# Kernel tuning notes

Hardware: AMD Instinct MI355X
Metric: run time of the kernel (lower is better)

The kernel has to match this reference:

```python
import jax, jax.numpy as jnp
import numpy as np

EPS = 1e-05
HEADS = 4

def rms_norm(x, w):
    norm = jax.lax.rsqrt(jnp.mean(x * x, axis=-1, keepdims=True) + EPS)
    return x * norm * w

def setup_inputs() -> dict:
    key = jax.random.key(0)
    ks = jax.random.split(key, 10)
    B, Nt, Nf, C = 2, 4096, 4096, 256
    s = 0.02
    return {
        "t": jax.random.normal(ks[0], (B, Nt, C), jnp.float32),
        "f": jax.random.normal(ks[1], (B, Nf, C), jnp.float32),
        "norm_w": jnp.ones((C,), jnp.float32),
        "wq": jax.random.normal(ks[2], (C, C), jnp.float32) * s,
        "bq": jnp.zeros((C,), jnp.float32),
        "wkv": jax.random.normal(ks[3], (C, 2 * C), jnp.float32) * s,
        "bkv": jnp.zeros((2 * C,), jnp.float32),
        "wp": jax.random.normal(ks[4], (C, C), jnp.float32) * s,
        "bp": jnp.zeros((C,), jnp.float32),
    }

def reference(t, f, norm_w, wq, bq, wkv, bkv, wp, bp):
    B, Nt, C = t.shape
    Nf = f.shape[1]
    H = HEADS
    Dh = C // H
    scale = Dh ** -0.5
    tn = rms_norm(t, norm_w)
    fn = rms_norm(f, norm_w)
    q = (tn @ wq + bq).reshape(B, Nt, H, Dh)          # b t h d
    kv = fn @ wkv + bkv
    k, v = jnp.split(kv, 2, axis=-1)
    k = k.reshape(B, Nf, H, Dh)                        # b f h d
    v = v.reshape(B, Nf, H, Dh)
    attn = jnp.einsum('bthd,bfhd->bhtf', q, k) * scale
    attn = jax.nn.softmax(attn, axis=-1)
    out = jnp.einsum('bhtf,bfhd->bthd', attn, v).reshape(B, Nt, C)
    return out @ wp + bp + tn
```

## Files before the change

kernel.cpp:

```cpp
#include <hip/hip_runtime.h>

typedef __bf16 bf16;
typedef __bf16 bf16x4 __attribute__((ext_vector_type(4)));
typedef __bf16 bf16x8 __attribute__((ext_vector_type(8)));
typedef float f32x2 __attribute__((ext_vector_type(2)));
typedef float f32x4 __attribute__((ext_vector_type(4)));
typedef float f32x16 __attribute__((ext_vector_type(16)));

__device__ __forceinline__ f32x4 mfma16(bf16x8 a, bf16x8 b, f32x4 c) {
  return __builtin_amdgcn_mfma_f32_16x16x32_bf16(a, b, c, 0, 0, 0);
}
__device__ __forceinline__ f32x16 mfma32(bf16x8 a, bf16x8 b, f32x16 c) {
  return __builtin_amdgcn_mfma_f32_32x32x16_bf16(a, b, c, 0, 0, 0);
}

__device__ __forceinline__ unsigned pack2(float lo, float hi) {
  unsigned short a = __builtin_bit_cast(unsigned short, (bf16)lo);
  unsigned short b = __builtin_bit_cast(unsigned short, (bf16)hi);
  return ((unsigned)b << 16) | (unsigned)a;
}

__device__ __forceinline__ void plane32swap(unsigned& a, unsigned& b) {
  asm volatile("v_permlane32_swap_b32 %0, %1" : "+v"(a), "+v"(b));
}

__device__ __forceinline__ f32x2 pk_add(f32x2 a, f32x2 b) {
  f32x2 d;
  asm("v_pk_add_f32 %0, %1, %2" : "=v"(d) : "v"(a), "v"(b));
  return d;
}

typedef __attribute__((address_space(3))) unsigned int lds_u32;
typedef __attribute__((address_space(1))) unsigned int glb_u32;
__device__ __forceinline__ void gld16(const bf16* g, bf16* l) {
  __builtin_amdgcn_global_load_lds((const glb_u32*)g, (lds_u32*)l, 16, 0, 0);
}

__global__ __launch_bounds__(256)
void prep_kernel(const float* __restrict__ t, const float* __restrict__ f,
                 const float* __restrict__ nw,
                 const float* __restrict__ wq, const float* __restrict__ wkv,
                 const float* __restrict__ wp,
                 bf16* __restrict__ tn, bf16* __restrict__ fn,
                 bf16* __restrict__ wqT, bf16* __restrict__ wkvT,
                 bf16* __restrict__ wpT)
{
  int b = blockIdx.x;
  if (b < 1024) {
    int e = b * 256 + threadIdx.x;
    const float* src; bf16* dst; int N; int idx;
    if (e < 65536)       { src = wq;  dst = wqT;  N = 256; idx = e; }
    else if (e < 196608) { src = wkv; dst = wkvT; N = 512; idx = e - 65536; }
    else                 { src = wp;  dst = wpT;  N = 256; idx = e - 196608; }
    int k = idx & 255;
    int n = idx >> 8;
    dst[idx] = (bf16)src[(size_t)k * N + n];
    return;
  }
  int wave = threadIdx.x >> 6;
  int lane = threadIdx.x & 63;
  int row = (b - 1024) * 4 + wave;
  const float* src;
  bf16* dst;
  if (row < 8192) {
    src = t + (size_t)row * 256;
    dst = tn + (size_t)row * 256;
  } else {
    int r2 = row - 8192;
    src = f + (size_t)r2 * 256;
    dst = fn + (size_t)r2 * 256;
  }
  float4 v = reinterpret_cast<const float4*>(src)[lane];
  float ss = v.x * v.x + v.y * v.y + v.z * v.z + v.w * v.w;
  #pragma unroll
  for (int m = 1; m < 64; m <<= 1) ss += __shfl_xor(ss, m);
  float nrm = rsqrtf(ss * (1.0f / 256.0f) + 1e-5f);
  float4 wv = reinterpret_cast<const float4*>(nw)[lane];
  bf16x4 o;
  o[0] = (bf16)(v.x * nrm * wv.x);
  o[1] = (bf16)(v.y * nrm * wv.y);
  o[2] = (bf16)(v.z * nrm * wv.z);
  o[3] = (bf16)(v.w * nrm * wv.w);
  *reinterpret_cast<bf16x4*>(dst + lane * 4) = o;
}

template<int MODE>
__device__ __forceinline__
void gemm_body(int bid, bf16 (*As)[264], bf16 (*Bs)[264],
               const bf16* __restrict__ A, const bf16* __restrict__ Wt,
               const float* __restrict__ bias, bf16* __restrict__ o0,
               bf16* __restrict__ o1, const bf16* __restrict__ resid,
               float* __restrict__ outf, int N)
{
  int tid = threadIdx.x;
  int wv = tid >> 6;
  int lane = tid & 63;
  int lr = lane & 15;
  int lk = (lane >> 4) * 8;
  int wm = wv >> 1, wn = wv & 1;
  int nb = N >> 6;
  int bm = bid / nb;
  int bn = bid - bm * nb;
  int row0 = bm * 64;
  int col0 = bn * 64;

  #pragma unroll
  for (int j = 0; j < 8; j++) {
    int idx = tid + 256 * j;
    int r = idx >> 5, ch = idx & 31;
    *reinterpret_cast<bf16x8*>(&As[r][ch * 8]) =
        *reinterpret_cast<const bf16x8*>(A + (size_t)(row0 + r) * 256 + ch * 8);
    *reinterpret_cast<bf16x8*>(&Bs[r][ch * 8]) =
        *reinterpret_cast<const bf16x8*>(Wt + (size_t)(col0 + r) * 256 + ch * 8);
  }
  __syncthreads();

  f32x4 acc[2][2] = {};
  #pragma unroll
  for (int k0 = 0; k0 < 256; k0 += 32) {
    bf16x8 a[2], b[2];
    #pragma unroll
    for (int mi = 0; mi < 2; mi++)
      a[mi] = *reinterpret_cast<const bf16x8*>(&As[wm * 32 + mi * 16 + lr][k0 + lk]);
    #pragma unroll
    for (int ni = 0; ni < 2; ni++)
      b[ni] = *reinterpret_cast<const bf16x8*>(&Bs[wn * 32 + ni * 16 + lr][k0 + lk]);
    #pragma unroll
    for (int mi = 0; mi < 2; mi++)
      #pragma unroll
      for (int ni = 0; ni < 2; ni++)
        acc[mi][ni] = mfma16(a[mi], b[ni], acc[mi][ni]);
  }

  int rb = (lane >> 4) * 4;
  int row0w = row0 + wm * 32;
  int col0w = col0 + wn * 32;
  #pragma unroll
  for (int mi = 0; mi < 2; mi++) {
    #pragma unroll
    for (int ni = 0; ni < 2; ni++) {
      int col = col0w + ni * 16 + lr;
      float bv = bias[col];
      #pragma unroll
      for (int r = 0; r < 4; r++) {
        int row = row0w + mi * 16 + rb + r;
        float val = acc[mi][ni][r] + bv;
        if (MODE == 0) {
          int b_ = row >> 12, tt = row & 4095;
          int h = col >> 6, d = col & 63;
          o0[(((size_t)(b_ * 4 + h)) * 4096 + tt) * 64 + d] = (bf16)val;
        } else if (MODE == 1) {
          int b_ = row >> 12, ff = row & 4095;
          if (col < 256) {
            int h = col >> 6, d = col & 63;
            o0[(((size_t)(b_ * 4 + h)) * 4096 + ff) * 64 + d] = (bf16)val;
          } else {
            int c = col - 256;
            int h = c >> 6, d = c & 63;
            o1[(((size_t)(b_ * 4 + h)) * 64 + d) * 4096 + ff] = (bf16)val;
          }
        } else {
          size_t idx = (size_t)row * 256 + col;
          outf[idx] = val + (float)resid[idx];
        }
      }
    }
  }
}

__global__ __launch_bounds__(256)
void gemm_qkv(const bf16* __restrict__ tn, const bf16* __restrict__ fn,
              const bf16* __restrict__ wqT, const bf16* __restrict__ wkvT,
              const float* __restrict__ bq, const float* __restrict__ bkv,
              bf16* __restrict__ q, bf16* __restrict__ k, bf16* __restrict__ vt)
{
  __shared__ bf16 As[64][264];
  __shared__ bf16 Bs[64][264];
  if (blockIdx.x < 512)
    gemm_body<0>(blockIdx.x, As, Bs, tn, wqT, bq, q, nullptr, nullptr, nullptr, 256);
  else
    gemm_body<1>(blockIdx.x - 512, As, Bs, fn, wkvT, bkv, k, vt, nullptr, nullptr, 512);
}

__global__ __launch_bounds__(256)
void gemm_out(const bf16* __restrict__ ao, const bf16* __restrict__ wpT,
              const float* __restrict__ bp, const bf16* __restrict__ resid,
              float* __restrict__ outf)
{
  __shared__ bf16 As[64][264];
  __shared__ bf16 Bs[64][264];
  gemm_body<2>(blockIdx.x, As, Bs, ao, wpT, bp, nullptr, nullptr, resid, outf, 256);
}

__global__ __launch_bounds__(128, 4)
void attn_kernel(const bf16* __restrict__ Q, const bf16* __restrict__ K,
                 const bf16* __restrict__ Vt, unsigned* __restrict__ Opart,
                 float* __restrict__ Lp)
{
  int bid = blockIdx.x;
  int bh = bid & 7;
  int qb = (bid >> 3) & 63;
  int FQ = bid >> 9;
  int wv = threadIdx.x >> 6;
  int lane = threadIdx.x & 63;
  int lq = lane & 31;
  int h32 = lane >> 5;

  const bf16* Qb = Q + ((size_t)bh * 4096 + qb * 64 + wv * 32) * 64;
  const bf16* Kb = K + (size_t)bh * 4096 * 64;
  const bf16* Vb = Vt + (size_t)bh * 64 * 4096;

  __shared__ bf16 stage[2][4096];

  const float qs = 0.125f * 1.44269504089f;
  bf16x8 qf[4];
  #pragma unroll
  for (int kc = 0; kc < 4; kc++) {
    qf[kc] = *reinterpret_cast<const bf16x8*>(Qb + (size_t)lq * 64 + kc * 16 + h32 * 8);
    #pragma unroll
    for (int i = 0; i < 8; i++) qf[kc][i] = (bf16)((float)qf[kc][i] * qs);
  }

  f32x16 zmm = {};
  f32x16 oa[2] = {};
  float l = 0.f;

  int fbeg = FQ * 1024;

  const bf16 *p0, *p1;
  if (wv == 0) {
    p0 = Kb + (size_t)(fbeg + lq) * 64 + h32 * 8;
    p1 = p0 + 32 * 64;
  } else {
    p0 = Vb + (size_t)lane * 4096 + fbeg;
    p1 = p0 + 32;
  }

  const bf16* kL0 = &stage[0][0] + h32 * 256 + lq * 8;
  const bf16* kL1 = &stage[1][0] + h32 * 256 + lq * 8;
  const bf16* vL0 = &stage[0][2048] + h32 * 512 + lq * 8;
  const bf16* vL1 = &stage[1][2048] + h32 * 512 + lq * 8;

  auto STAGE = [&](bf16* sb, const bf16* p) {
    if (wv == 0) {
      gld16(p,      sb);
      gld16(p + 16, sb + 512);
      gld16(p + 32, sb + 1024);
      gld16(p + 48, sb + 1536);
    } else {
      gld16(p,      sb + 2048);
      gld16(p + 8,  sb + 2560);
      gld16(p + 16, sb + 3072);
      gld16(p + 24, sb + 3584);
    }
  };

  auto BODY = [&](const bf16* kL, const bf16* vL) {
    asm volatile("s_waitcnt vmcnt(4)" ::: "memory");
    __builtin_amdgcn_s_barrier();
    asm volatile("" ::: "memory");

    f32x16 st = mfma32(*reinterpret_cast<const bf16x8*>(kL),        qf[0], zmm);
    st        = mfma32(*reinterpret_cast<const bf16x8*>(kL + 512),  qf[1], st);
    st        = mfma32(*reinterpret_cast<const bf16x8*>(kL + 1024), qf[2], st);
    st        = mfma32(*reinterpret_cast<const bf16x8*>(kL + 1536), qf[3], st);

    union { f32x2 p2[8]; float s[16]; } u;
    #pragma unroll
    for (int r = 0; r < 16; r++) u.s[r] = exp2f(st[r]);

    f32x2 a0 = pk_add(u.p2[0], u.p2[1]);
    f32x2 a1 = pk_add(u.p2[2], u.p2[3]);
    f32x2 a2 = pk_add(u.p2[4], u.p2[5]);
    f32x2 a3 = pk_add(u.p2[6], u.p2[7]);
    a0 = pk_add(a0, a1);
    a2 = pk_add(a2, a3);
    a0 = pk_add(a0, a2);
    l += a0[0] + a0[1];

    unsigned w[8];
    #pragma unroll
    for (int j = 0; j < 8; j++) w[j] = pack2(u.s[2 * j], u.s[2 * j + 1]);
    plane32swap(w[0], w[2]);
    plane32swap(w[1], w[3]);
    plane32swap(w[4], w[6]);
    plane32swap(w[5], w[7]);
    union { unsigned u4[4]; bf16x8 v; } ub0, ub1;
    ub0.u4[0] = w[0]; ub0.u4[1] = w[1]; ub0.u4[2] = w[2]; ub0.u4[3] = w[3];
    ub1.u4[0] = w[4]; ub1.u4[1] = w[5]; ub1.u4[2] = w[6]; ub1.u4[3] = w[7];

    oa[0] = mfma32(*reinterpret_cast<const bf16x8*>(vL),        ub0.v, oa[0]);
    oa[0] = mfma32(*reinterpret_cast<const bf16x8*>(vL + 1024), ub1.v, oa[0]);
    oa[1] = mfma32(*reinterpret_cast<const bf16x8*>(vL + 256),  ub0.v, oa[1]);
    oa[1] = mfma32(*reinterpret_cast<const bf16x8*>(vL + 1280), ub1.v, oa[1]);

    asm volatile("" ::: "memory");
    __builtin_amdgcn_s_barrier();
    asm volatile("" ::: "memory");
  };

  STAGE(&stage[0][0], p0);
  STAGE(&stage[1][0], p1);
  asm volatile("" ::: "memory");

  const int adv = (wv == 0) ? 64 * 64 : 64;
  #pragma unroll 1
  for (int u = 0; u < 16; ++u) {
    BODY(kL0, vL0);
    p0 += adv;
    STAGE(&stage[0][0], p0);
    asm volatile("" ::: "memory");
    BODY(kL1, vL1);
    p1 += adv;
    STAGE(&stage[1][0], p1);
    asm volatile("" ::: "memory");
  }

  asm volatile("s_waitcnt vmcnt(0)" ::: "memory");

  float ltot;
  {
    unsigned x = __builtin_bit_cast(unsigned, l), y = x;
    plane32swap(x, y);
    ltot = __builtin_bit_cast(float, x) + __builtin_bit_cast(float, y);
  }

  unsigned* op = Opart + (((size_t)(FQ * 8 + bh) * 128 + qb * 2 + wv) * 1024);
  #pragma unroll
  for (int db = 0; db < 2; db++)
    #pragma unroll
    for (int j = 0; j < 8; j++) {
      int r = 2 * j;
      int d = db * 32 + 2 * (j & 1) + 8 * (j >> 1) + 4 * h32;
      op[(d >> 1) * 32 + lq] = pack2(oa[db][r], oa[db][r + 1]);
    }
  if (h32 == 0)
    Lp[((size_t)FQ * 8 + bh) * 4096 + qb * 64 + wv * 32 + lq] = ltot;
}

__global__ __launch_bounds__(256)
void merge_kernel(const unsigned* __restrict__ Op, const float* __restrict__ Lp,
                  bf16* __restrict__ AO)
{
  int bid = blockIdx.x;
  int bh = bid & 7;
  int tile = bid >> 3;
  int tid = threadIdx.x;
  int q = tid & 31;
  int c4 = tid >> 5;
  int row0 = tile * 32;

  float L = 0.f;
  #pragma unroll
  for (int p = 0; p < 4; p++)
    L += Lp[((size_t)p * 8 + bh) * 4096 + row0 + q];
  float inv = 1.f / L;

  __shared__ unsigned tl[32][33];
  float a0[4] = {}, a1[4] = {};
  #pragma unroll
  for (int p = 0; p < 4; p++) {
    const unsigned* src = Op + (((size_t)p * 8 + bh) * 128 + tile) * 1024;
    #pragma unroll
    for (int j = 0; j < 4; j++) {
      unsigned v = src[(c4 + j * 8) * 32 + q];
      a0[j] += (float)__builtin_bit_cast(bf16, (unsigned short)(v & 0xffff));
      a1[j] += (float)__builtin_bit_cast(bf16, (unsigned short)(v >> 16));
    }
  }
  #pragma unroll
  for (int j = 0; j < 4; j++)
    tl[q][c4 + j * 8] = pack2(a0[j] * inv, a1[j] * inv);
  __syncthreads();

  int q2 = tid >> 3;
  int dg = tid & 7;
  unsigned ov[4];
  #pragma unroll
  for (int i = 0; i < 4; i++) ov[i] = tl[q2][dg * 4 + i];
  int b_ = bh >> 2, hh = bh & 3;
  int row = row0 + q2;
  unsigned* dst = (unsigned*)(AO + ((size_t)b_ * 4096 + row) * 256 + hh * 64) + dg * 4;
  *reinterpret_cast<uint4*>(dst) = *reinterpret_cast<const uint4*>(ov);
}

extern "C" void kernel_launch(void* const* d_in, const int* in_sizes, int n_in,
                              void* d_out, int out_size, void* d_ws, size_t ws_size,
                              hipStream_t stream) {
  const float* t   = (const float*)d_in[0];
  const float* f   = (const float*)d_in[1];
  const float* nw  = (const float*)d_in[2];
  const float* wq  = (const float*)d_in[3];
  const float* bq  = (const float*)d_in[4];
  const float* wkv = (const float*)d_in[5];
  const float* bkv = (const float*)d_in[6];
  const float* wp  = (const float*)d_in[7];
  const float* bp  = (const float*)d_in[8];
  float* out = (float*)d_out;

  bf16* ws = (bf16*)d_ws;
  const size_t NTOK = 2097152;
  bf16* tn   = ws;
  bf16* fn   = ws + NTOK;
  bf16* q    = ws + 2 * NTOK;
  bf16* k    = ws + 3 * NTOK;
  bf16* vt   = ws + 4 * NTOK;
  bf16* ao   = fn;
  bf16* wqT  = ws + 5 * NTOK;
  bf16* wkvT = wqT + 65536;
  bf16* wpT  = wkvT + 131072;
  unsigned* opart = (unsigned*)(wpT + 65536);
  float* lp = (float*)(opart + (size_t)4 * 8 * 128 * 1024);

  prep_kernel<<<5120, 256, 0, stream>>>(t, f, nw, wq, wkv, wp, tn, fn, wqT, wkvT, wpT);
  gemm_qkv<<<1536, 256, 0, stream>>>(tn, fn, wqT, wkvT, bq, bkv, q, k, vt);
  attn_kernel<<<2048, 128, 0, stream>>>(q, k, vt, opart, lp);
  merge_kernel<<<1024, 256, 0, stream>>>(opart, lp, ao);
  gemm_out<<<512, 256, 0, stream>>>(ao, wpT, bp, tn, out);
}
```

Measured before the change: 110.8 us.

## Widen attention blocks to four waves sharing K/V staging, split keys eight ways

Each attention block now holds four waves covering 128 query rows instead of two covering 64, and all four waves share the staging of K and V tiles, so every wave issues two loads per stage instead of four. The key dimension is split into eight partitions of 512 instead of four of 1024, which keeps the grid at 2048 blocks. The goal is to halve K/V global and LDS staging traffic per query row and spread the loads across more waves. In exchange the merge kernel reads twice as many partial outputs, and the partial buffer doubles in size.

```diff
diff --git a/kernel.cpp b/kernel.cpp
--- a/kernel.cpp
+++ b/kernel.cpp
@@ -192,21 +192,21 @@
   gemm_body<2>(blockIdx.x, As, Bs, ao, wpT, bp, nullptr, nullptr, resid, outf, 256);
 }
 
-__global__ __launch_bounds__(128, 4)
+__global__ __launch_bounds__(256, 4)
 void attn_kernel(const bf16* __restrict__ Q, const bf16* __restrict__ K,
                  const bf16* __restrict__ Vt, unsigned* __restrict__ Opart,
                  float* __restrict__ Lp)
 {
   int bid = blockIdx.x;
   int bh = bid & 7;
-  int qb = (bid >> 3) & 63;
-  int FQ = bid >> 9;
+  int qb = (bid >> 3) & 31;
+  int FQ = bid >> 8;
   int wv = threadIdx.x >> 6;
   int lane = threadIdx.x & 63;
   int lq = lane & 31;
   int h32 = lane >> 5;
 
-  const bf16* Qb = Q + ((size_t)bh * 4096 + qb * 64 + wv * 32) * 64;
+  const bf16* Qb = Q + ((size_t)bh * 4096 + qb * 128 + wv * 32) * 64;
   const bf16* Kb = K + (size_t)bh * 4096 * 64;
   const bf16* Vb = Vt + (size_t)bh * 64 * 4096;
 
@@ -225,16 +225,21 @@
   f32x16 oa[2] = {};
   float l = 0.f;
 
-  int fbeg = FQ * 1024;
-
+  int fbeg = FQ * 512;
+
+  int role = wv >> 1;
+  int half = wv & 1;
   const bf16 *p0, *p1;
-  if (wv == 0) {
-    p0 = Kb + (size_t)(fbeg + lq) * 64 + h32 * 8;
+  if (role == 0) {
+    p0 = Kb + (size_t)(fbeg + lq) * 64 + h32 * 8 + half * 32;
     p1 = p0 + 32 * 64;
   } else {
-    p0 = Vb + (size_t)lane * 4096 + fbeg;
+    p0 = Vb + (size_t)lane * 4096 + fbeg + half * 16;
     p1 = p0 + 32;
   }
+  const int so  = role ? 8 : 16;
+  const int adv = role ? 64 : 64 * 64;
+  const int db0 = wv * 1024;
 
   const bf16* kL0 = &stage[0][0] + h32 * 256 + lq * 8;
   const bf16* kL1 = &stage[1][0] + h32 * 256 + lq * 8;
@@ -242,21 +247,12 @@
   const bf16* vL1 = &stage[1][2048] + h32 * 512 + lq * 8;
 
   auto STAGE = [&](bf16* sb, const bf16* p) {
-    if (wv == 0) {
-      gld16(p,      sb);
-      gld16(p + 16, sb + 512);
-      gld16(p + 32, sb + 1024);
-      gld16(p + 48, sb + 1536);
-    } else {
-      gld16(p,      sb + 2048);
-      gld16(p + 8,  sb + 2560);
-      gld16(p + 16, sb + 3072);
-      gld16(p + 24, sb + 3584);
-    }
+    gld16(p,      sb + db0);
+    gld16(p + so, sb + db0 + 512);
   };
 
   auto BODY = [&](const bf16* kL, const bf16* vL) {
-    asm volatile("s_waitcnt vmcnt(4)" ::: "memory");
+    asm volatile("s_waitcnt vmcnt(2)" ::: "memory");
     __builtin_amdgcn_s_barrier();
     asm volatile("" ::: "memory");
 
@@ -303,9 +299,8 @@
   STAGE(&stage[1][0], p1);
   asm volatile("" ::: "memory");
 
-  const int adv = (wv == 0) ? 64 * 64 : 64;
   #pragma unroll 1
-  for (int u = 0; u < 16; ++u) {
+  for (int u = 0; u < 8; ++u) {
     BODY(kL0, vL0);
     p0 += adv;
     STAGE(&stage[0][0], p0);
@@ -325,7 +320,8 @@
     ltot = __builtin_bit_cast(float, x) + __builtin_bit_cast(float, y);
   }
 
-  unsigned* op = Opart + (((size_t)(FQ * 8 + bh) * 128 + qb * 2 + wv) * 1024);
+  int tile = qb * 4 + wv;
+  unsigned* op = Opart + (((size_t)(FQ * 8 + bh) * 128 + tile) * 1024);
   #pragma unroll
   for (int db = 0; db < 2; db++)
     #pragma unroll
@@ -335,7 +331,7 @@
       op[(d >> 1) * 32 + lq] = pack2(oa[db][r], oa[db][r + 1]);
     }
   if (h32 == 0)
-    Lp[((size_t)FQ * 8 + bh) * 4096 + qb * 64 + wv * 32 + lq] = ltot;
+    Lp[((size_t)FQ * 8 + bh) * 4096 + tile * 32 + lq] = ltot;
 }
 
 __global__ __launch_bounds__(256)
@@ -352,14 +348,14 @@
 
   float L = 0.f;
   #pragma unroll
-  for (int p = 0; p < 4; p++)
+  for (int p = 0; p < 8; p++)
     L += Lp[((size_t)p * 8 + bh) * 4096 + row0 + q];
   float inv = 1.f / L;
 
   __shared__ unsigned tl[32][33];
   float a0[4] = {}, a1[4] = {};
   #pragma unroll
-  for (int p = 0; p < 4; p++) {
+  for (int p = 0; p < 8; p++) {
     const unsigned* src = Op + (((size_t)p * 8 + bh) * 128 + tile) * 1024;
     #pragma unroll
     for (int j = 0; j < 4; j++) {
@@ -410,11 +406,11 @@
   bf16* wkvT = wqT + 65536;
   bf16* wpT  = wkvT + 131072;
   unsigned* opart = (unsigned*)(wpT + 65536);
-  float* lp = (float*)(opart + (size_t)4 * 8 * 128 * 1024);
+  float* lp = (float*)(opart + (size_t)8 * 8 * 128 * 1024);
 
   prep_kernel<<<5120, 256, 0, stream>>>(t, f, nw, wq, wkv, wp, tn, fn, wqT, wkvT, wpT);
   gemm_qkv<<<1536, 256, 0, stream>>>(tn, fn, wqT, wkvT, bq, bkv, q, k, vt);
-  attn_kernel<<<2048, 128, 0, stream>>>(q, k, vt, opart, lp);
+  attn_kernel<<<2048, 256, 0, stream>>>(q, k, vt, opart, lp);
   merge_kernel<<<1024, 256, 0, stream>>>(opart, lp, ao);
   gemm_out<<<512, 256, 0, stream>>>(ao, wpT, bp, tn, out);
 }
```

After: 99.39 us. 10.3% less time.

## Process two query tiles per wave and split keys eight ways in attention

Applied to the files above, without the earlier changes.

Each attention wave now handles 64 query rows, as two 32-row tiles, against every staged K/V chunk. This doubles reuse of each LDS-staged key/value tile and halves the number of staging barriers per unit of work. To keep the grid the same size, the key range is split into 8 partitions instead of 4, so the merge kernel sums more partials and the partial buffer doubles. Launch bounds drop to 3 blocks per CU to allow for the extra registers, and the bf16 packing of probabilities now uses a single hardware convert-pack instruction.

```diff
diff --git a/kernel.cpp b/kernel.cpp
--- a/kernel.cpp
+++ b/kernel.cpp
@@ -18,6 +18,12 @@
   unsigned short a = __builtin_bit_cast(unsigned short, (bf16)lo);
   unsigned short b = __builtin_bit_cast(unsigned short, (bf16)hi);
   return ((unsigned)b << 16) | (unsigned)a;
+}
+
+__device__ __forceinline__ unsigned cvtpk(float lo, float hi) {
+  unsigned r;
+  asm("v_cvt_pk_bf16_f32 %0, %1, %2" : "=v"(r) : "v"(lo), "v"(hi));
+  return r;
 }
 
 __device__ __forceinline__ void plane32swap(unsigned& a, unsigned& b) {
@@ -192,40 +198,44 @@
   gemm_body<2>(blockIdx.x, As, Bs, ao, wpT, bp, nullptr, nullptr, resid, outf, 256);
 }
 
-__global__ __launch_bounds__(128, 4)
+__global__ __launch_bounds__(128, 3)
 void attn_kernel(const bf16* __restrict__ Q, const bf16* __restrict__ K,
                  const bf16* __restrict__ Vt, unsigned* __restrict__ Opart,
                  float* __restrict__ Lp)
 {
   int bid = blockIdx.x;
   int bh = bid & 7;
-  int qb = (bid >> 3) & 63;
-  int FQ = bid >> 9;
+  int qb = (bid >> 3) & 31;
+  int FQ = bid >> 8;
   int wv = threadIdx.x >> 6;
   int lane = threadIdx.x & 63;
   int lq = lane & 31;
   int h32 = lane >> 5;
 
-  const bf16* Qb = Q + ((size_t)bh * 4096 + qb * 64 + wv * 32) * 64;
+  const bf16* Qw = Q + ((size_t)bh * 4096 + qb * 128 + wv * 64) * 64;
   const bf16* Kb = K + (size_t)bh * 4096 * 64;
   const bf16* Vb = Vt + (size_t)bh * 64 * 4096;
 
   __shared__ bf16 stage[2][4096];
 
   const float qs = 0.125f * 1.44269504089f;
-  bf16x8 qf[4];
+  bf16x8 qfA[4], qfB[4];
   #pragma unroll
   for (int kc = 0; kc < 4; kc++) {
-    qf[kc] = *reinterpret_cast<const bf16x8*>(Qb + (size_t)lq * 64 + kc * 16 + h32 * 8);
-    #pragma unroll
-    for (int i = 0; i < 8; i++) qf[kc][i] = (bf16)((float)qf[kc][i] * qs);
+    qfA[kc] = *reinterpret_cast<const bf16x8*>(Qw + (size_t)lq * 64 + kc * 16 + h32 * 8);
+    qfB[kc] = *reinterpret_cast<const bf16x8*>(Qw + (size_t)(32 + lq) * 64 + kc * 16 + h32 * 8);
+    #pragma unroll
+    for (int i = 0; i < 8; i++) {
+      qfA[kc][i] = (bf16)((float)qfA[kc][i] * qs);
+      qfB[kc][i] = (bf16)((float)qfB[kc][i] * qs);
+    }
   }
 
   f32x16 zmm = {};
-  f32x16 oa[2] = {};
-  float l = 0.f;
-
-  int fbeg = FQ * 1024;
+  f32x16 oaA[2] = {}, oaB[2] = {};
+  float lA = 0.f, lB = 0.f;
+
+  int fbeg = FQ * 512;
 
   const bf16 *p0, *p1;
   if (wv == 0) {
@@ -235,6 +245,7 @@
     p0 = Vb + (size_t)lane * 4096 + fbeg;
     p1 = p0 + 32;
   }
+  const int adv = (wv == 0) ? 64 * 64 : 64;
 
   const bf16* kL0 = &stage[0][0] + h32 * 256 + lq * 8;
   const bf16* kL1 = &stage[1][0] + h32 * 256 + lq * 8;
@@ -255,17 +266,14 @@
     }
   };
 
-  auto BODY = [&](const bf16* kL, const bf16* vL) {
-    asm volatile("s_waitcnt vmcnt(4)" ::: "memory");
-    __builtin_amdgcn_s_barrier();
-    asm volatile("" ::: "memory");
-
+  auto TILE = [&](const bf16* kL, const bf16* vL, const bf16x8* qf,
+                  f32x16* oa, float& l) {
     f32x16 st = mfma32(*reinterpret_cast<const bf16x8*>(kL),        qf[0], zmm);
     st        = mfma32(*reinterpret_cast<const bf16x8*>(kL + 512),  qf[1], st);
     st        = mfma32(*reinterpret_cast<const bf16x8*>(kL + 1024), qf[2], st);
     st        = mfma32(*reinterpret_cast<const bf16x8*>(kL + 1536), qf[3], st);
 
-    union { f32x2 p2[8]; float s[16]; } u;
+    union { f32x16 v; f32x2 p2[8]; float s[16]; } u;
     #pragma unroll
     for (int r = 0; r < 16; r++) u.s[r] = exp2f(st[r]);
 
@@ -280,7 +288,7 @@
 
     unsigned w[8];
     #pragma unroll
-    for (int j = 0; j < 8; j++) w[j] = pack2(u.s[2 * j], u.s[2 * j + 1]);
+    for (int j = 0; j < 8; j++) w[j] = cvtpk(u.s[2 * j], u.s[2 * j + 1]);
     plane32swap(w[0], w[2]);
     plane32swap(w[1], w[3]);
     plane32swap(w[4], w[6]);
@@ -293,7 +301,14 @@
     oa[0] = mfma32(*reinterpret_cast<const bf16x8*>(vL + 1024), ub1.v, oa[0]);
     oa[1] = mfma32(*reinterpret_cast<const bf16x8*>(vL + 256),  ub0.v, oa[1]);
     oa[1] = mfma32(*reinterpret_cast<const bf16x8*>(vL + 1280), ub1.v, oa[1]);
-
+  };
+
+  auto BODY = [&](const bf16* kL, const bf16* vL) {
+    asm volatile("s_waitcnt vmcnt(4)" ::: "memory");
+    __builtin_amdgcn_s_barrier();
+    asm volatile("" ::: "memory");
+    TILE(kL, vL, qfA, oaA, lA);
+    TILE(kL, vL, qfB, oaB, lB);
     asm volatile("" ::: "memory");
     __builtin_amdgcn_s_barrier();
     asm volatile("" ::: "memory");
@@ -303,9 +318,8 @@
   STAGE(&stage[1][0], p1);
   asm volatile("" ::: "memory");
 
-  const int adv = (wv == 0) ? 64 * 64 : 64;
   #pragma unroll 1
-  for (int u = 0; u < 16; ++u) {
+  for (int u = 0; u < 8; ++u) {
     BODY(kL0, vL0);
     p0 += adv;
     STAGE(&stage[0][0], p0);
@@ -318,24 +332,29 @@
 
   asm volatile("s_waitcnt vmcnt(0)" ::: "memory");
 
-  float ltot;
-  {
-    unsigned x = __builtin_bit_cast(unsigned, l), y = x;
-    plane32swap(x, y);
-    ltot = __builtin_bit_cast(float, x) + __builtin_bit_cast(float, y);
-  }
-
-  unsigned* op = Opart + (((size_t)(FQ * 8 + bh) * 128 + qb * 2 + wv) * 1024);
-  #pragma unroll
-  for (int db = 0; db < 2; db++)
-    #pragma unroll
-    for (int j = 0; j < 8; j++) {
-      int r = 2 * j;
-      int d = db * 32 + 2 * (j & 1) + 8 * (j >> 1) + 4 * h32;
-      op[(d >> 1) * 32 + lq] = pack2(oa[db][r], oa[db][r + 1]);
+  int tile0 = qb * 4 + wv * 2;
+  #pragma unroll
+  for (int s = 0; s < 2; s++) {
+    f32x16* oa = s ? oaB : oaA;
+    float l = s ? lB : lA;
+    float ltot;
+    {
+      unsigned x = __builtin_bit_cast(unsigned, l), y = x;
+      plane32swap(x, y);
+      ltot = __builtin_bit_cast(float, x) + __builtin_bit_cast(float, y);
     }
-  if (h32 == 0)
-    Lp[((size_t)FQ * 8 + bh) * 4096 + qb * 64 + wv * 32 + lq] = ltot;
+    unsigned* op = Opart + (((size_t)(FQ * 8 + bh) * 128 + tile0 + s) * 1024);
+    #pragma unroll
+    for (int db = 0; db < 2; db++)
+      #pragma unroll
+      for (int j = 0; j < 8; j++) {
+        int r = 2 * j;
+        int d = db * 32 + 2 * (j & 1) + 8 * (j >> 1) + 4 * h32;
+        op[(d >> 1) * 32 + lq] = pack2(oa[db][r], oa[db][r + 1]);
+      }
+    if (h32 == 0)
+      Lp[((size_t)FQ * 8 + bh) * 4096 + (tile0 + s) * 32 + lq] = ltot;
+  }
 }
 
 __global__ __launch_bounds__(256)
@@ -352,14 +371,14 @@
 
   float L = 0.f;
   #pragma unroll
-  for (int p = 0; p < 4; p++)
+  for (int p = 0; p < 8; p++)
     L += Lp[((size_t)p * 8 + bh) * 4096 + row0 + q];
   float inv = 1.f / L;
 
   __shared__ unsigned tl[32][33];
   float a0[4] = {}, a1[4] = {};
   #pragma unroll
-  for (int p = 0; p < 4; p++) {
+  for (int p = 0; p < 8; p++) {
     const unsigned* src = Op + (((size_t)p * 8 + bh) * 128 + tile) * 1024;
     #pragma unroll
     for (int j = 0; j < 4; j++) {
@@ -410,7 +429,7 @@
   bf16* wkvT = wqT + 65536;
   bf16* wpT  = wkvT + 131072;
   unsigned* opart = (unsigned*)(wpT + 65536);
-  float* lp = (float*)(opart + (size_t)4 * 8 * 128 * 1024);
+  float* lp = (float*)(opart + (size_t)8 * 8 * 128 * 1024);
 
   prep_kernel<<<5120, 256, 0, stream>>>(t, f, nw, wq, wkv, wp, tn, fn, wqT, wkvT, wpT);
   gemm_qkv<<<1536, 256, 0, stream>>>(tn, fn, wqT, wkvT, bq, bkv, q, k, vt);
```

Measured after the change: 110.8 us. Within noise of the previous version (-0.0%).
